# Kernel optimization log

Measured on AMD Instinct MI355X. Metric: run time of the kernel, lower is better.

The kernel has to match this reference:

```python
import jax, jax.numpy as jnp
import numpy as np

B = 128          # batch
H = 4            # input_size (number of local blocks / heads)
SEQ = 256        # seq_length
E = 64           # embedding_size
D = 64           # qkv_size
LH = SEQ // H    # seq_length_head = 64
NEG = -1e20

def setup_inputs() -> dict:
    key = jax.random.key(0)
    ks = jax.random.split(key, 7)
    scale = 0.02
    sequence = jax.random.normal(ks[0], (B, SEQ, E), dtype=jnp.float32)
    WQ = jax.random.normal(ks[1], (H, LH * D, LH * E), dtype=jnp.float32) * scale
    WK = jax.random.normal(ks[2], (H, LH * D, LH * E), dtype=jnp.float32) * scale
    WV = jax.random.normal(ks[3], (H, LH * D, LH * E), dtype=jnp.float32) * scale
    bQ = jax.random.normal(ks[4], (H, LH * D), dtype=jnp.float32) * scale
    bK = jax.random.normal(ks[5], (H, LH * D), dtype=jnp.float32) * scale
    bV = jax.random.normal(ks[6], (H, LH * D), dtype=jnp.float32) * scale
    return {"sequence": sequence, "WQ": WQ, "bQ": bQ, "WK": WK, "bK": bK, "WV": WV, "bV": bV}

def reference(sequence, WQ, bQ, WK, bK, WV, bV):
    b = sequence.shape[0]
    # split sequence into H independent local blocks, flatten each block
    x = sequence.reshape(b, H, LH * E)  # [B, H, Lh*E]
    # per-block dense projections (flattened linears, as in the original)
    Q = (jnp.einsum('bhi,hoi->bho', x, WQ) + bQ).reshape(b, H, LH, D)
    K = (jnp.einsum('bhi,hoi->bho', x, WK) + bK).reshape(b, H, LH, D)
    V = (jnp.einsum('bhi,hoi->bho', x, WV) + bV).reshape(b, H, LH, D)
    scores = jnp.einsum('bhqd,bhkd->bhqk', Q, K)  # [B, H, Lh, Lh]
    # masked=True: add -1e20 above the diagonal (as in torch.triu(..., diagonal=1))
    mask = jnp.triu(jnp.full((LH, LH), NEG, dtype=scores.dtype), k=1)
    scores = scores + mask
    # FAITHFUL to original: nn.Softmax(dim=1) on [B, Lh, Lh] -> softmax over QUERY axis
    attn = jax.nn.softmax(scores, axis=2)
    Z = jnp.einsum('bhqk,bhkd->bhqd', attn, V) * (1.0 / jnp.sqrt(jnp.float32(D)))
    return Z.reshape(b, SEQ, D)
```

## Files before the change

kernel.cpp:

```cpp
#include <hip/hip_runtime.h>

typedef _Float16 half8 __attribute__((ext_vector_type(8)));
typedef float floatx16 __attribute__((ext_vector_type(16)));

#define B_   128
#define H_   4
#define SEQ_ 256
#define E_   64
#define D_   64
#define LH_  64
#define IN_  (LH_*E_)
#define OUT_ (LH_*D_)
#define QKV_MAT_ELEMS (B_*H_*OUT_)

__device__ __forceinline__ half8 cvt8(float4 lo, float4 hi) {
    half8 v;
    v[0] = (_Float16)lo.x; v[1] = (_Float16)lo.y;
    v[2] = (_Float16)lo.z; v[3] = (_Float16)lo.w;
    v[4] = (_Float16)hi.x; v[5] = (_Float16)hi.y;
    v[6] = (_Float16)hi.z; v[7] = (_Float16)hi.w;
    return v;
}

__global__ __launch_bounds__(128) void qkv_gemm(
    const float* __restrict__ seq,
    const float* __restrict__ WQ, const float* __restrict__ bQ,
    const float* __restrict__ WK, const float* __restrict__ bK,
    const float* __restrict__ WV, const float* __restrict__ bV,
    _Float16* __restrict__ qkv)
{
    const int i   = blockIdx.x;
    const int h   = (i >> 1) & 3;
    const int sub = (i & 1) + ((i >> 3) << 1);
    const int mat = sub >> 6;
    const int nt  = sub & 63;
    const int o0  = nt * 64;

    const float* __restrict__ W    = (mat == 0) ? WQ : (mat == 1) ? WK : WV;
    const float* __restrict__ bias = (mat == 0) ? bQ : (mat == 1) ? bK : bV;

    const int wave = threadIdx.x >> 6;
    const int lane = threadIdx.x & 63;
    const int lrow = lane & 31;
    const int kg   = lane >> 5;
    const int m0   = wave * 64;

    const float* xr0 = seq + (size_t)(m0 + lrow) * (SEQ_*E_) + (size_t)h * IN_ + kg * 8;
    const float* xr1 = xr0 + (size_t)32 * (SEQ_*E_);
    const float* wr0 = W + (size_t)h * IN_ * OUT_ + (size_t)(o0 + lrow) * IN_ + kg * 8;
    const float* wr1 = wr0 + (size_t)32 * IN_;

    floatx16 acc00, acc01, acc10, acc11;
    #pragma unroll
    for (int r = 0; r < 16; ++r) { acc00[r]=0.f; acc01[r]=0.f; acc10[r]=0.f; acc11[r]=0.f; }

    for (int kt = 0; kt < 64; ++kt) {
        #pragma unroll
        for (int s = 0; s < 4; ++s) {
            const int k = kt * 64 + s * 16;
            float4 a0l = *(const float4*)(xr0 + k);
            float4 a0h = *(const float4*)(xr0 + k + 4);
            float4 a1l = *(const float4*)(xr1 + k);
            float4 a1h = *(const float4*)(xr1 + k + 4);
            float4 b0l = *(const float4*)(wr0 + k);
            float4 b0h = *(const float4*)(wr0 + k + 4);
            float4 b1l = *(const float4*)(wr1 + k);
            float4 b1h = *(const float4*)(wr1 + k + 4);
            half8 a0 = cvt8(a0l, a0h);
            half8 a1 = cvt8(a1l, a1h);
            half8 b0 = cvt8(b0l, b0h);
            half8 b1 = cvt8(b1l, b1h);
            acc00 = __builtin_amdgcn_mfma_f32_32x32x16_f16(a0, b0, acc00, 0, 0, 0);
            acc01 = __builtin_amdgcn_mfma_f32_32x32x16_f16(a0, b1, acc01, 0, 0, 0);
            acc10 = __builtin_amdgcn_mfma_f32_32x32x16_f16(a1, b0, acc10, 0, 0, 0);
            acc11 = __builtin_amdgcn_mfma_f32_32x32x16_f16(a1, b1, acc11, 0, 0, 0);
        }
    }

    const float bv0 = bias[(size_t)h * OUT_ + o0 + lrow];
    const float bv1 = bias[(size_t)h * OUT_ + o0 + 32 + lrow];
    _Float16* dst = qkv + (size_t)mat * QKV_MAT_ELEMS;
    #pragma unroll
    for (int r = 0; r < 16; ++r) {
        const int row = (r & 3) + 8 * (r >> 2) + 4 * kg;
        const int b0r = m0 + row;
        const int b1r = m0 + 32 + row;
        size_t i0 = ((size_t)(b0r * H_ + h)) * OUT_ + o0;
        size_t i1 = ((size_t)(b1r * H_ + h)) * OUT_ + o0;
        dst[i0 + lrow]      = (_Float16)(acc00[r] + bv0);
        dst[i0 + 32 + lrow] = (_Float16)(acc01[r] + bv1);
        dst[i1 + lrow]      = (_Float16)(acc10[r] + bv0);
        dst[i1 + 32 + lrow] = (_Float16)(acc11[r] + bv1);
    }
}

__global__ __launch_bounds__(256) void local_attn(
    const _Float16* __restrict__ qkv, float* __restrict__ out)
{
    __shared__ half8 Pf[64 * 8];
    __shared__ half8 Vt[64 * 8];
    __shared__ float redM[2][64];
    __shared__ float redS[2][64];
    __shared__ float invL[64];

    const int t = threadIdx.x;
    const int h = blockIdx.x;
    const int b = blockIdx.y;
    const size_t base = ((size_t)(b * H_ + h)) * OUT_;

    const _Float16* Q = qkv + base;
    const _Float16* K = qkv + (size_t)QKV_MAT_ELEMS + base;
    const _Float16* V = qkv + (size_t)2 * QKV_MAT_ELEMS + base;

    half8 v0 = *(const half8*)(V + (size_t)t * 8);
    half8 v1 = *(const half8*)(V + (size_t)(t + 256) * 8);

    const int wave = t >> 6, lane = t & 63;
    const int lrow = lane & 31, kg = lane >> 5;
    const int qt = wave >> 1, kt = wave & 1;

    floatx16 s;
    #pragma unroll
    for (int r = 0; r < 16; ++r) s[r] = 0.f;
    #pragma unroll
    for (int st = 0; st < 4; ++st) {
        half8 a  = *(const half8*)(Q + (qt * 32 + lrow) * 64 + st * 16 + kg * 8);
        half8 bb = *(const half8*)(K + (kt * 32 + lrow) * 64 + st * 16 + kg * 8);
        s = __builtin_amdgcn_mfma_f32_32x32x16_f16(a, bb, s, 0, 0, 0);
    }

    const int col = kt * 32 + lrow;
    float m = -3.4e38f;
    #pragma unroll
    for (int r = 0; r < 16; ++r) {
        const int q = qt * 32 + (r & 3) + 8 * (r >> 2) + 4 * kg;
        if (col > q) s[r] = -1e20f;
        m = fmaxf(m, s[r]);
    }
    m = fmaxf(m, __shfl_xor(m, 32));
    redM[qt][col] = m;
    __syncthreads();
    m = fmaxf(redM[0][col], redM[1][col]);

    float sum = 0.f;
    #pragma unroll
    for (int r = 0; r < 16; ++r) {
        float e = __expf(s[r] - m);
        s[r] = e;
        sum += e;
    }
    sum += __shfl_xor(sum, 32);
    redS[qt][col] = sum;
    __syncthreads();
    const float inv = 1.f / (redS[0][col] + redS[1][col]);
    if (qt == 0 && kg == 0) invL[col] = inv * 0.125f;

    {
        _Float16* p = (_Float16*)Pf;
        const int k8 = col >> 3;
        #pragma unroll
        for (int r = 0; r < 16; ++r) {
            const int q = qt * 32 + (r & 3) + 8 * (r >> 2) + 4 * kg;
            p[(q * 8 + (k8 ^ (q & 7))) * 8 + (col & 7)] = (_Float16)s[r];
        }
    }
    __syncthreads();

    {
        _Float16* vt = (_Float16*)Vt;
        const int k0 = t >> 3, d80 = t & 7;
        const float iv0 = invL[k0];
        #pragma unroll
        for (int j = 0; j < 8; ++j) {
            const int d = d80 * 8 + j;
            vt[(d * 8 + ((k0 >> 3) ^ (d & 7))) * 8 + (k0 & 7)] = (_Float16)((float)v0[j] * iv0);
        }
        const int k1 = (t + 256) >> 3;
        const float iv1 = invL[k1];
        #pragma unroll
        for (int j = 0; j < 8; ++j) {
            const int d = d80 * 8 + j;
            vt[(d * 8 + ((k1 >> 3) ^ (d & 7))) * 8 + (k1 & 7)] = (_Float16)((float)v1[j] * iv1);
        }
    }
    __syncthreads();

    const int dt = kt;
    floatx16 z;
    #pragma unroll
    for (int r = 0; r < 16; ++r) z[r] = 0.f;
    #pragma unroll
    for (int st = 0; st < 4; ++st) {
        const int k8 = st * 2 + kg;
        const int q  = qt * 32 + lrow;
        const int d  = dt * 32 + lrow;
        half8 a  = Pf[q * 8 + (k8 ^ (q & 7))];
        half8 bb = Vt[d * 8 + (k8 ^ (d & 7))];
        z = __builtin_amdgcn_mfma_f32_32x32x16_f16(a, bb, z, 0, 0, 0);
    }
    #pragma unroll
    for (int r = 0; r < 16; ++r) {
        const int q = qt * 32 + (r & 3) + 8 * (r >> 2) + 4 * kg;
        const int d = dt * 32 + lrow;
        out[((size_t)b * SEQ_ + h * LH_ + q) * D_ + d] = z[r];
    }
}

extern "C" void kernel_launch(void* const* d_in, const int* in_sizes, int n_in,
                              void* d_out, int out_size, void* d_ws, size_t ws_size,
                              hipStream_t stream)
{
    const float* seq = (const float*)d_in[0];
    const float* WQ  = (const float*)d_in[1];
    const float* bQ  = (const float*)d_in[2];
    const float* WK  = (const float*)d_in[3];
    const float* bK  = (const float*)d_in[4];
    const float* WV  = (const float*)d_in[5];
    const float* bV  = (const float*)d_in[6];
    _Float16* qkv = (_Float16*)d_ws;
    float* out = (float*)d_out;

    qkv_gemm<<<768, 128, 0, stream>>>(seq, WQ, bQ, WK, bK, WV, bV, qkv);
    dim3 g2(H_, B_);
    local_attn<<<g2, 256, 0, stream>>>(qkv, out);
}
```

Baseline: 956.1 us.

## Stage weight tiles through LDS with async triple-buffered global_load_lds

The QKV GEMM now uses 256 threads per block, with each wave owning 32 batch rows instead of 64. The 64x64 weight tile is loaded once per block into LDS through a triple-buffered global_load_lds pipeline, synchronised with waitcnt and barrier. Previously each wave reloaded the weight rows straight from global memory. This is meant to cut redundant weight traffic and overlap loads with MFMA work, at the cost of about 50KB of LDS per block, a barrier every k-tile, and hand-tuned waitcnt values.

```diff
diff --git a/kernel.cpp b/kernel.cpp
--- a/kernel.cpp
+++ b/kernel.cpp
@@ -13,6 +13,9 @@
 #define OUT_ (LH_*D_)
 #define QKV_MAT_ELEMS (B_*H_*OUT_)
 
+#define UNIT_B  1040
+#define STAGE_B (16 * UNIT_B)
+
 __device__ __forceinline__ half8 cvt8(float4 lo, float4 hi) {
     half8 v;
     v[0] = (_Float16)lo.x; v[1] = (_Float16)lo.y;
@@ -22,13 +25,15 @@
     return v;
 }
 
-__global__ __launch_bounds__(128) void qkv_gemm(
+__global__ __launch_bounds__(256, 3) void qkv_gemm(
     const float* __restrict__ seq,
     const float* __restrict__ WQ, const float* __restrict__ bQ,
     const float* __restrict__ WK, const float* __restrict__ bK,
     const float* __restrict__ WV, const float* __restrict__ bV,
     _Float16* __restrict__ qkv)
 {
+    __shared__ alignas(16) char smem[3 * STAGE_B];
+
     const int i   = blockIdx.x;
     const int h   = (i >> 1) & 3;
     const int sub = (i & 1) + ((i >> 3) << 1);
@@ -38,42 +43,74 @@
 
     const float* __restrict__ W    = (mat == 0) ? WQ : (mat == 1) ? WK : WV;
     const float* __restrict__ bias = (mat == 0) ? bQ : (mat == 1) ? bK : bV;
-
-    const int wave = threadIdx.x >> 6;
-    const int lane = threadIdx.x & 63;
+    const float* __restrict__ Wblk = W + (size_t)h * IN_ * OUT_ + (size_t)o0 * IN_;
+
+    const int t    = threadIdx.x;
+    const int wave = t >> 6;
+    const int lane = t & 63;
     const int lrow = lane & 31;
     const int kg   = lane >> 5;
-    const int m0   = wave * 64;
-
-    const float* xr0 = seq + (size_t)(m0 + lrow) * (SEQ_*E_) + (size_t)h * IN_ + kg * 8;
-    const float* xr1 = xr0 + (size_t)32 * (SEQ_*E_);
-    const float* wr0 = W + (size_t)h * IN_ * OUT_ + (size_t)(o0 + lrow) * IN_ + kg * 8;
-    const float* wr1 = wr0 + (size_t)32 * IN_;
-
-    floatx16 acc00, acc01, acc10, acc11;
-    #pragma unroll
-    for (int r = 0; r < 16; ++r) { acc00[r]=0.f; acc01[r]=0.f; acc10[r]=0.f; acc11[r]=0.f; }
+
+    const int dmarow_sub = lane >> 4;
+    const int dmacol     = (lane & 15) * 4;
+
+    const float* xr = seq + (size_t)(wave * 32 + lrow) * (SEQ_ * E_)
+                          + (size_t)h * IN_ + kg * 8;
+
+    floatx16 acc0, acc1;
+    #pragma unroll
+    for (int r = 0; r < 16; ++r) { acc0[r] = 0.f; acc1[r] = 0.f; }
+
+    auto issue = [&](int ktile, int buf) {
+        char* sb = smem + buf * STAGE_B;
+        #pragma unroll
+        for (int j = 0; j < 4; ++j) {
+            const int u   = j * 4 + wave;
+            const int row = u * 4 + dmarow_sub;
+            const float* g = Wblk + (size_t)row * IN_ + ktile * 64 + dmacol;
+            __builtin_amdgcn_global_load_lds(
+                (const __attribute__((address_space(1))) void*)g,
+                (__attribute__((address_space(3))) void*)(sb + u * UNIT_B),
+                16, 0, 0);
+        }
+    };
+
+    issue(0, 0);
+    issue(1, 1);
+
+    const int fragoff = (lrow >> 2) * UNIT_B + (lrow & 3) * 256 + kg * 32;
 
     for (int kt = 0; kt < 64; ++kt) {
-        #pragma unroll
-        for (int s = 0; s < 4; ++s) {
-            const int k = kt * 64 + s * 16;
-            float4 a0l = *(const float4*)(xr0 + k);
-            float4 a0h = *(const float4*)(xr0 + k + 4);
-            float4 a1l = *(const float4*)(xr1 + k);
-            float4 a1h = *(const float4*)(xr1 + k + 4);
-            float4 b0l = *(const float4*)(wr0 + k);
-            float4 b0h = *(const float4*)(wr0 + k + 4);
-            float4 b1l = *(const float4*)(wr1 + k);
-            float4 b1h = *(const float4*)(wr1 + k + 4);
-            half8 a0 = cvt8(a0l, a0h);
-            half8 a1 = cvt8(a1l, a1h);
-            half8 b0 = cvt8(b0l, b0h);
-            half8 b1 = cvt8(b1l, b1h);
-            acc00 = __builtin_amdgcn_mfma_f32_32x32x16_f16(a0, b0, acc00, 0, 0, 0);
-            acc01 = __builtin_amdgcn_mfma_f32_32x32x16_f16(a0, b1, acc01, 0, 0, 0);
-            acc10 = __builtin_amdgcn_mfma_f32_32x32x16_f16(a1, b0, acc10, 0, 0, 0);
-            acc11 = __builtin_amdgcn_mfma_f32_32x32x16_f16(a1, b1, acc11, 0, 0, 0);
+        __atomic_signal_fence(__ATOMIC_ACQ_REL);
+        __builtin_amdgcn_s_waitcnt(0xF74);
+        __builtin_amdgcn_s_barrier();
+        __atomic_signal_fence(__ATOMIC_ACQ_REL);
+
+        const float* xk = xr + kt * 64;
+        float4 a[8];
+        #pragma unroll
+        for (int s2 = 0; s2 < 4; ++s2) {
+            a[2 * s2]     = *(const float4*)(xk + s2 * 16);
+            a[2 * s2 + 1] = *(const float4*)(xk + s2 * 16 + 4);
+        }
+
+        issue((kt + 2 <= 63) ? kt + 2 : 63, (kt + 2) % 3);
+        __atomic_signal_fence(__ATOMIC_ACQ_REL);
+
+        const char* stb = smem + (kt % 3) * STAGE_B + fragoff;
+        #pragma unroll
+        for (int s2 = 0; s2 < 4; ++s2) {
+            half8 af = cvt8(a[2 * s2], a[2 * s2 + 1]);
+            const char* p0 = stb + s2 * 64;
+            const char* p1 = p0 + 8 * UNIT_B;
+            float4 b0l = *(const float4*)p0;
+            float4 b0h = *(const float4*)(p0 + 16);
+            float4 b1l = *(const float4*)p1;
+            float4 b1h = *(const float4*)(p1 + 16);
+            half8 bf0 = cvt8(b0l, b0h);
+            half8 bf1 = cvt8(b1l, b1h);
+            acc0 = __builtin_amdgcn_mfma_f32_32x32x16_f16(af, bf0, acc0, 0, 0, 0);
+            acc1 = __builtin_amdgcn_mfma_f32_32x32x16_f16(af, bf1, acc1, 0, 0, 0);
         }
     }
 
@@ -83,14 +120,10 @@
     #pragma unroll
     for (int r = 0; r < 16; ++r) {
         const int row = (r & 3) + 8 * (r >> 2) + 4 * kg;
-        const int b0r = m0 + row;
-        const int b1r = m0 + 32 + row;
-        size_t i0 = ((size_t)(b0r * H_ + h)) * OUT_ + o0;
-        size_t i1 = ((size_t)(b1r * H_ + h)) * OUT_ + o0;
-        dst[i0 + lrow]      = (_Float16)(acc00[r] + bv0);
-        dst[i0 + 32 + lrow] = (_Float16)(acc01[r] + bv1);
-        dst[i1 + lrow]      = (_Float16)(acc10[r] + bv0);
-        dst[i1 + 32 + lrow] = (_Float16)(acc11[r] + bv1);
+        const int b   = wave * 32 + row;
+        size_t idx = ((size_t)(b * H_ + h)) * OUT_ + o0;
+        dst[idx + lrow]      = (_Float16)(acc0[r] + bv0);
+        dst[idx + 32 + lrow] = (_Float16)(acc1[r] + bv1);
     }
 }
 
@@ -220,7 +253,7 @@
     _Float16* qkv = (_Float16*)d_ws;
     float* out = (float*)d_out;
 
-    qkv_gemm<<<768, 128, 0, stream>>>(seq, WQ, bQ, WK, bK, WV, bV, qkv);
+    qkv_gemm<<<768, 256, 0, stream>>>(seq, WQ, bQ, WK, bK, WV, bV, qkv);
     dim3 g2(H_, B_);
     local_attn<<<g2, 256, 0, stream>>>(qkv, out);
 }
```

Measured after the change: 798.2 us. -16.5%, faster.
